# Optimization experiments

Measured on AMD Instinct MI355X. Metric: run time of the kernel, lower is better.

## Reference

```python
import jax, jax.numpy as jnp
import numpy as np

B, N, D, H, K, NH = 4096, 2048, 1024, 4096, 5, 8
HD = D // NH  # head dim


def setup_inputs() -> dict:
    key = jax.random.key(0)
    ks = jax.random.split(key, 12)
    s_d = np.float32(1.0 / np.sqrt(D))
    s_h = np.float32(1.0 / np.sqrt(H))
    rn = lambda k, sh, s: jax.random.normal(k, sh, dtype=jnp.float32) * s
    return {
        "morph0": jax.random.normal(ks[0], (B, D), dtype=jnp.float32),
        "stored_morph0": jax.random.normal(ks[1], (N, D), dtype=jnp.float32),
        "stored_morph1": jax.random.normal(ks[2], (N, D), dtype=jnp.float32),
        "wq": rn(ks[3], (D, D), s_d), "bq": jnp.zeros((D,), jnp.float32),
        "wk": rn(ks[4], (D, D), s_d), "bk": jnp.zeros((D,), jnp.float32),
        "wv": rn(ks[5], (D, D), s_d), "bv": jnp.zeros((D,), jnp.float32),
        "wo": rn(ks[6], (D, D), s_d), "bo": jnp.zeros((D,), jnp.float32),
        "w1": rn(ks[7], (H, D), s_d), "b1": jnp.zeros((H,), jnp.float32),
        "w2": rn(ks[8], (H, H), s_h), "b2": jnp.zeros((H,), jnp.float32),
        "w3": rn(ks[9], (D, H), s_h), "b3": jnp.zeros((D,), jnp.float32),
    }


def _l2norm(x):
    # F.normalize(dim=1): x / max(||x||, eps)
    n = jnp.sqrt(jnp.sum(x * x, axis=-1, keepdims=True))
    return x / jnp.maximum(n, 1e-12)


def reference(morph0, stored_morph0, stored_morph1,
              wq, bq, wk, bk, wv, bv, wo, bo,
              w1, b1, w2, b2, w3, b3):
    # ---- retrieve similar patterns: cosine sim + topk + fused gather-subtract ----
    qn = _l2norm(morph0)                       # [B, D]
    sn = _l2norm(stored_morph0)                # [N, D]
    sim = qn @ sn.T                            # [B, N]
    _, top_idx = jax.lax.top_k(sim, K)         # [B, K]
    evo = stored_morph1 - stored_morph0        # [N, D]
    selected = jnp.take(evo, top_idx, axis=0)  # [B, K, D] evolution vectors

    # ---- torch.nn.MultiheadAttention(D, 8, batch_first=True), eval mode ----
    q = (morph0 @ wq.T + bq).reshape(B, 1, NH, HD)      # [B, 1, NH, HD]
    k = (selected @ wk.T + bk).reshape(B, K, NH, HD)    # [B, K, NH, HD]
    v = (selected @ wv.T + bv).reshape(B, K, NH, HD)
    scores = jnp.einsum('bqhd,bkhd->bhqk', q, k) / np.float32(np.sqrt(HD))  # [B, NH, 1, K]
    attn = jax.nn.softmax(scores, axis=-1)
    ctx = jnp.einsum('bhqk,bkhd->bqhd', attn, v).reshape(B, 1, D)
    context = (ctx @ wo.T + bo)[:, 0, :]                # [B, D]
    attn_weights = attn.mean(axis=1)                    # [B, 1, K] (avg over heads)

    # ---- evolution net (dropout inactive in eval) + residual ----
    x = morph0 + context
    h1 = jax.nn.relu(x @ w1.T + b1)
    h2 = jax.nn.relu(h1 @ w2.T + b2)
    predicted = morph0 + (h2 @ w3.T + b3)
    return predicted, attn_weights
```

## Files before the change

### kernel.cpp

```cpp
#include <hip/hip_runtime.h>
#include <hip/hip_bf16.h>
#include <math.h>

typedef __bf16 bf16_t;
typedef __bf16 bf16x4 __attribute__((ext_vector_type(4)));
typedef __bf16 bf16x8 __attribute__((ext_vector_type(8)));
typedef float  f32x4  __attribute__((ext_vector_type(4)));

#define BB 4096
#define NN 2048
#define DD 1024
#define HH 4096
#define KSEL 5
#define NHEAD 8

__device__ __forceinline__ unsigned short bfbits(float f) {
  return __builtin_bit_cast(unsigned short, (bf16_t)f);
}

__device__ __forceinline__ void gload_lds16(const void* g, void* l) {
  __builtin_amdgcn_global_load_lds(
      (const __attribute__((address_space(1))) void*)g,
      (__attribute__((address_space(3))) void*)l, 16, 0, 0);
}

__device__ __forceinline__ ushort4 cvt4(float4 x) {
  ushort4 o;
  o.x = bfbits(x.x); o.y = bfbits(x.y); o.z = bfbits(x.z); o.w = bfbits(x.w);
  return o;
}

#define P_M0   1048576
#define P_S0   1572864
#define P_EVO  2097152
#define P_WQ   2359296
#define P_WKV  2883584
#define P_WO   3145728
#define P_W1   4194304
#define P_W2   8388608
#define P_W3   9437184
#define P_BKV  9437696
__global__ void __launch_bounds__(256)
prep_k(const float4* __restrict__ m0, const float4* __restrict__ s0,
       const float4* __restrict__ s1,
       const float4* __restrict__ wq, const float4* __restrict__ wk,
       const float4* __restrict__ wv, const float4* __restrict__ wo,
       const float4* __restrict__ w1, const float4* __restrict__ w2,
       const float4* __restrict__ w3,
       const float4* __restrict__ bk, const float4* __restrict__ bv,
       ushort4* __restrict__ m0b, ushort4* __restrict__ s0b,
       ushort4* __restrict__ evo,
       ushort4* __restrict__ wqb, ushort4* __restrict__ wkvb,
       ushort4* __restrict__ wob,
       ushort4* __restrict__ w1b, ushort4* __restrict__ w2b,
       ushort4* __restrict__ w3b, float4* __restrict__ bkv,
       double* __restrict__ rnd)
{
  __shared__ double red[256];
  const int tid = threadIdx.x;
  if (blockIdx.x >= 2048) {
    int n = blockIdx.x - 2048;
    float4 x = s0[(size_t)n * 256 + tid];
    double ss = (double)x.x * x.x + (double)x.y * x.y + (double)x.z * x.z + (double)x.w * x.w;
    red[tid] = ss; __syncthreads();
    for (int s = 128; s > 0; s >>= 1) {
      if (tid < s) red[tid] += red[tid + s];
      __syncthreads();
    }
    if (tid == 0) rnd[n] = 1.0 / fmax(sqrt(red[0]), 1e-12);
    return;
  }
  const int stride = 2048 * 256;
  for (int i = blockIdx.x * 256 + tid; i < P_BKV; i += stride) {
    if (i < P_M0) {
      m0b[i] = cvt4(m0[i]);
    } else if (i < P_S0) {
      int j = i - P_M0; s0b[j] = cvt4(s0[j]);
    } else if (i < P_EVO) {
      int j = i - P_S0;
      float4 a = s0[j], b = s1[j];
      float4 d; d.x = b.x - a.x; d.y = b.y - a.y; d.z = b.z - a.z; d.w = b.w - a.w;
      evo[j] = cvt4(d);
    } else if (i < P_WQ) {
      int j = i - P_EVO; wqb[j] = cvt4(wq[j]);
    } else if (i < P_WKV) {
      int j = i - P_WQ;
      wkvb[j] = cvt4(j < 262144 ? wk[j] : wv[j - 262144]);
    } else if (i < P_WO) {
      int j = i - P_WKV; wob[j] = cvt4(wo[j]);
    } else if (i < P_W1) {
      int j = i - P_WO; w1b[j] = cvt4(w1[j]);
    } else if (i < P_W2) {
      int j = i - P_W1; w2b[j] = cvt4(w2[j]);
    } else if (i < P_W3) {
      int j = i - P_W2; w3b[j] = cvt4(w3[j]);
    } else {
      int j = i - P_W3;
      bkv[j] = (j < 256) ? bk[j] : bv[j - 256];
    }
  }
}

template<bool RELU, bool RESID, bool OUTBF16>
__global__ void __launch_bounds__(256)
gemm_bt(const bf16_t* __restrict__ A, const bf16_t* __restrict__ Bw,
        const float* __restrict__ bias, const float* __restrict__ resid,
        float* __restrict__ outf, bf16_t* __restrict__ outb,
        int M, int Nn, int Kk)
{
  __shared__ alignas(16) bf16_t At[2][4096];
  __shared__ alignas(16) bf16_t Bt[2][4096];
  const int tid = threadIdx.x;
  const int wave = tid >> 6, lane = tid & 63;
  const int wm = wave >> 1, wn = wave & 1;
  const int bm = blockIdx.y << 7, bn = blockIdx.x << 7;
  const int ln15 = lane & 15, ln4 = lane >> 4;

  const int srow  = (wave << 4) + (lane >> 2);
  const int scolb = (((lane & 3) ^ ((lane >> 3) & 3)) << 4);
  const char* pA0 = (const char*)A  + (size_t)(bm + srow) * Kk * 2 + scolb;
  const char* pA1 = (const char*)A  + (size_t)(bm + srow + 64) * Kk * 2 + scolb;
  const char* pB0 = (const char*)Bw + (size_t)(bn + srow) * Kk * 2 + scolb;
  const char* pB1 = (const char*)Bw + (size_t)(bn + srow + 64) * Kk * 2 + scolb;

  f32x4 zero = {0.f, 0.f, 0.f, 0.f};
  f32x4 acc[4][4];
  #pragma unroll
  for (int i = 0; i < 4; ++i)
    #pragma unroll
    for (int j = 0; j < 4; ++j) acc[i][j] = zero;

  const int rslot = (ln4 ^ ((ln15 >> 1) & 3)) << 3;
  const int fAoff = ((wm << 6) + ln15) * 32 + rslot;
  const int fBoff = ((wn << 6) + ln15) * 32 + rslot;

  const int nt = Kk >> 5;
  {
    char* lA = (char*)At[0] + (wave << 10);
    char* lB = (char*)Bt[0] + (wave << 10);
    gload_lds16(pA0, lA);
    gload_lds16(pA1, lA + 4096);
    gload_lds16(pB0, lB);
    gload_lds16(pB1, lB + 4096);
  }
  __syncthreads();

  for (int t = 0; t < nt; ++t) {
    const int cur = t & 1;
    if (t + 1 < nt) {
      size_t kb = (size_t)(t + 1) << 6;
      char* lA = (char*)At[cur ^ 1] + (wave << 10);
      char* lB = (char*)Bt[cur ^ 1] + (wave << 10);
      gload_lds16(pA0 + kb, lA);
      gload_lds16(pA1 + kb, lA + 4096);
      gload_lds16(pB0 + kb, lB);
      gload_lds16(pB1 + kb, lB + 4096);
    }
    bf16x8 av[4], bv[4];
    #pragma unroll
    for (int i = 0; i < 4; ++i) av[i] = *(const bf16x8*)(&At[cur][fAoff + i * 512]);
    #pragma unroll
    for (int j = 0; j < 4; ++j) bv[j] = *(const bf16x8*)(&Bt[cur][fBoff + j * 512]);
    #pragma unroll
    for (int i = 0; i < 4; ++i)
      #pragma unroll
      for (int j = 0; j < 4; ++j)
        acc[i][j] = __builtin_amdgcn_mfma_f32_16x16x32_bf16(av[i], bv[j], acc[i][j], 0, 0, 0);
    __syncthreads();
  }

  const int r0 = bm + (wm << 6) + ((lane >> 4) << 2);
  const int c0 = bn + (wn << 6) + ln15;
  #pragma unroll
  for (int i = 0; i < 4; ++i) {
    #pragma unroll
    for (int j = 0; j < 4; ++j) {
      #pragma unroll
      for (int r = 0; r < 4; ++r) {
        int row = r0 + i * 16 + r;
        int col = c0 + j * 16;
        size_t o = (size_t)row * Nn + col;
        float v = acc[i][j][r];
        if (bias)  v += bias[col];
        if (RESID) v += resid[o];
        if (RELU)  v = fmaxf(v, 0.f);
        if (OUTBF16) outb[o] = (bf16_t)v;
        else         outf[o] = v;
      }
    }
  }
}

template<bool RELU>
__global__ void __launch_bounds__(512, 2)
gemm8(const bf16_t* __restrict__ A, const bf16_t* __restrict__ Bw,
      const float* __restrict__ bias, bf16_t* __restrict__ outb,
      int Nn, int Kk, int nbx)
{
  __shared__ alignas(16) bf16_t As[2][2][8192];
  __shared__ alignas(16) bf16_t Bs[2][2][8192];
  const int lane = threadIdx.x & 63, wv = threadIdx.x >> 6;
  const int wm = wv >> 2, wn = wv & 3;
  const int ln15 = lane & 15, ln4 = lane >> 4;

  const int nwg = gridDim.x;
  const int q = nwg >> 3, r = nwg & 7;
  const int xcd = blockIdx.x & 7, loc = blockIdx.x >> 3;
  const int swz = (xcd < r ? xcd * (q + 1) : r * (q + 1) + (xcd - r) * q) + loc;
  const int bm = (swz / nbx) << 8;
  const int bn = (swz % nbx) << 8;

  const int NT = Kk >> 6;

  f32x4 acc[8][4];
  f32x4 zero = {0.f, 0.f, 0.f, 0.f};
  #pragma unroll
  for (int i = 0; i < 8; ++i)
    #pragma unroll
    for (int j = 0; j < 4; ++j) acc[i][j] = zero;

  auto stA = [&](int mh, int buf, int kt) {
    #pragma unroll
    for (int u = 0; u < 2; ++u) {
      int lr = u * 64 + wv * 8 + (lane >> 3);
      int gr = ((lr >> 6) << 7) | (mh << 6) | (lr & 63);
      int slot = (lane & 7) ^ (lr & 7);
      gload_lds16(A + (size_t)(bm + gr) * Kk + kt * 64 + slot * 8,
                  (char*)&As[buf][mh][0] + (u * 64 + wv * 8) * 128);
    }
  };
  auto stB = [&](int nh, int buf, int kt) {
    #pragma unroll
    for (int u = 0; u < 2; ++u) {
      int lr = u * 64 + wv * 8 + (lane >> 3);
      int gr = ((lr >> 5) << 6) | (nh << 5) | (lr & 31);
      int slot = (lane & 7) ^ (lr & 7);
      gload_lds16(Bw + (size_t)(bn + gr) * Kk + kt * 64 + slot * 8,
                  (char*)&Bs[buf][nh][0] + (u * 64 + wv * 8) * 128);
    }
  };

  stB(0, 0, 0); stA(1, 0, 0); stB(1, 0, 0); stA(0, 0, 0);
  stB(0, 1, 1); stA(1, 1, 1); stB(1, 1, 1);
  asm volatile("s_waitcnt vmcnt(6)" ::: "memory");
  __builtin_amdgcn_s_barrier();

#define RD_A(MH, BF)                                                              \
    _Pragma("unroll") for (int mi = 0; mi < 4; ++mi)                              \
      _Pragma("unroll") for (int kk = 0; kk < 2; ++kk) {                          \
        const int lr = wm * 64 + mi * 16 + ln15;                                  \
        avv[mi][kk] = *(const bf16x8*)((const char*)&As[BF][MH][0] + lr * 128 +   \
                                       ((((kk << 2) | ln4) ^ (ln15 & 7)) << 4));  \
      }
#define RD_B(NH, BF)                                                              \
    _Pragma("unroll") for (int nj = 0; nj < 2; ++nj)                              \
      _Pragma("unroll") for (int kk = 0; kk < 2; ++kk) {                          \
        const int lr = wn * 32 + nj * 16 + ln15;                                  \
        bvv[nj][kk] = *(const bf16x8*)((const char*)&Bs[BF][NH][0] + lr * 128 +   \
                                       ((((kk << 2) | ln4) ^ (ln15 & 7)) << 4));  \
      }
#define GATE                                                                      \
    __builtin_amdgcn_s_barrier();                                                 \
    asm volatile("s_waitcnt lgkmcnt(0)" ::: "memory");                            \
    __builtin_amdgcn_sched_barrier(0);
#define MMA(MH, NH)                                                               \
    __builtin_amdgcn_s_setprio(1);                                                \
    _Pragma("unroll") for (int kk = 0; kk < 2; ++kk)                              \
      _Pragma("unroll") for (int mi = 0; mi < 4; ++mi)                            \
        _Pragma("unroll") for (int nj = 0; nj < 2; ++nj)                          \
          acc[(MH)*4+mi][(NH)*2+nj] = __builtin_amdgcn_mfma_f32_16x16x32_bf16(    \
              avv[mi][kk], bvv[nj][kk], acc[(MH)*4+mi][(NH)*2+nj], 0, 0, 0);      \
    __builtin_amdgcn_s_setprio(0);                                                \
    __builtin_amdgcn_s_barrier();

  for (int base = 0; base < NT; base += 2) {
    const bool more = (base + 2 < NT);
    bf16x8 avv[4][2], bvv[2][2];

    RD_A(0, 0); RD_B(0, 0);
    stA(0, 1, base + 1);
    asm volatile("s_waitcnt lgkmcnt(8)");
    GATE; MMA(0, 0);
    RD_A(1, 0);
    if (more) stB(0, 0, base + 2);
    GATE; MMA(1, 0);
    RD_B(1, 0);
    if (more) stA(1, 0, base + 2);
    GATE; MMA(1, 1);
    RD_A(0, 0);
    if (more) {
      stB(1, 0, base + 2);
      asm volatile("s_waitcnt vmcnt(6)" ::: "memory");
    } else {
      asm volatile("s_waitcnt vmcnt(0)" ::: "memory");
    }
    GATE; MMA(0, 1);

    RD_A(0, 1); RD_B(0, 1);
    if (more) stA(0, 0, base + 2);
    asm volatile("s_waitcnt lgkmcnt(8)");
    GATE; MMA(0, 0);
    RD_A(1, 1);
    if (more) stB(0, 1, base + 3);
    GATE; MMA(1, 0);
    RD_B(1, 1);
    if (more) stA(1, 1, base + 3);
    GATE; MMA(1, 1);
    RD_A(0, 1);
    if (more) stB(1, 1, base + 3);
    asm volatile("s_waitcnt vmcnt(6)" ::: "memory");
    GATE; MMA(0, 1);
  }
#undef RD_A
#undef RD_B
#undef GATE
#undef MMA

  #pragma unroll
  for (int am = 0; am < 8; ++am) {
    #pragma unroll
    for (int an = 0; an < 4; ++an) {
      #pragma unroll
      for (int rr = 0; rr < 4; ++rr) {
        int row = bm + wm * 128 + (am >> 2) * 64 + (am & 3) * 16 + (lane >> 4) * 4 + rr;
        int col = bn + wn * 64 + (an >> 1) * 32 + (an & 1) * 16 + ln15;
        float v = acc[am][an][rr] + bias[col];
        if (RELU) v = fmaxf(v, 0.f);
        outb[(size_t)row * Nn + col] = (bf16_t)v;
      }
    }
  }
}

__global__ void __launch_bounds__(256)
topk_refine_k(const float* __restrict__ sim, const double* __restrict__ rnd,
              const float* __restrict__ m0, const float* __restrict__ s0,
              int* __restrict__ topidx)
{
  __shared__ float vals[NN];
  __shared__ float rv[256];
  __shared__ int   ri[256];
  __shared__ int   c8[8];
  __shared__ double dred[256];
  __shared__ double dvals[8];
  const int b = blockIdx.x, tid = threadIdx.x;
  for (int t = 0; t < NN / 256; ++t) {
    int i = tid + t * 256;
    vals[i] = sim[(size_t)b * NN + i] * (float)rnd[i];
  }
  __syncthreads();
  for (int p = 0; p < 8; ++p) {
    float bvv = -INFINITY; int bi = NN;
    for (int t = 0; t < NN / 256; ++t) {
      int i = tid + t * 256;
      float v = vals[i];
      if (v > bvv) { bvv = v; bi = i; }
    }
    rv[tid] = bvv; ri[tid] = bi;
    __syncthreads();
    for (int s = 128; s > 0; s >>= 1) {
      if (tid < s) {
        float v2 = rv[tid + s]; int i2 = ri[tid + s];
        if (v2 > rv[tid] || (v2 == rv[tid] && i2 < ri[tid])) { rv[tid] = v2; ri[tid] = i2; }
      }
      __syncthreads();
    }
    if (tid == 0) {
      int wsel = ri[0];
      c8[p] = wsel;
      vals[wsel] = -INFINITY;
    }
    __syncthreads();
  }
  int cs[8];
  #pragma unroll
  for (int j = 0; j < 8; ++j) cs[j] = c8[j];
  const float* qrow = m0 + (size_t)b * DD;
  double part[8];
  #pragma unroll
  for (int j = 0; j < 8; ++j) part[j] = 0.0;
  for (int d = tid; d < DD; d += 256) {
    double qd = (double)qrow[d];
    #pragma unroll
    for (int j = 0; j < 8; ++j)
      part[j] += qd * (double)s0[(size_t)cs[j] * DD + d];
  }
  for (int j = 0; j < 8; ++j) {
    dred[tid] = part[j]; __syncthreads();
    for (int s = 128; s > 0; s >>= 1) {
      if (tid < s) dred[tid] += dred[tid + s];
      __syncthreads();
    }
    if (tid == 0) dvals[j] = dred[0] * rnd[cs[j]];
    __syncthreads();
  }
  if (tid == 0) {
    bool used[8] = {false,false,false,false,false,false,false,false};
    for (int p = 0; p < KSEL; ++p) {
      int best = -1;
      for (int j = 0; j < 8; ++j) {
        if (used[j]) continue;
        if (best < 0 || dvals[j] > dvals[best] ||
            (dvals[j] == dvals[best] && cs[j] < cs[best])) best = j;
      }
      used[best] = true;
      topidx[b * KSEL + p] = cs[best];
    }
  }
}

__global__ void __launch_bounds__(256)
attn_k(const bf16_t* __restrict__ q, const bf16_t* __restrict__ eKV,
       const int* __restrict__ tidx,
       bf16_t* __restrict__ ctx, float* __restrict__ attn_out)
{
  __shared__ float aw[NHEAD][KSEL];
  const int b = blockIdx.x, t = threadIdx.x;
  const int d0 = t << 2;
  int idx[KSEL];
  #pragma unroll
  for (int j = 0; j < KSEL; ++j) idx[j] = tidx[b * KSEL + j];

  bf16x4 qv = *(const bf16x4*)(q + (size_t)b * DD + d0);
  float s[KSEL];
  #pragma unroll
  for (int j = 0; j < KSEL; ++j) {
    bf16x4 kv = *(const bf16x4*)(eKV + (size_t)idx[j] * 2048 + d0);
    float p = (float)qv[0] * (float)kv[0] + (float)qv[1] * (float)kv[1]
            + (float)qv[2] * (float)kv[2] + (float)qv[3] * (float)kv[3];
    #pragma unroll
    for (int m = 16; m > 0; m >>= 1) p += __shfl_xor(p, m);
    s[j] = p * 0.08838834764831845f;
  }
  float mx = s[0];
  #pragma unroll
  for (int j = 1; j < KSEL; ++j) mx = fmaxf(mx, s[j]);
  float e[KSEL], sum = 0.f;
  #pragma unroll
  for (int j = 0; j < KSEL; ++j) { e[j] = expf(s[j] - mx); sum += e[j]; }
  float inv = 1.f / sum;

  float c0 = 0.f, c1 = 0.f, c2 = 0.f, c3 = 0.f;
  #pragma unroll
  for (int j = 0; j < KSEL; ++j) {
    float a = e[j] * inv;
    bf16x4 vv = *(const bf16x4*)(eKV + (size_t)idx[j] * 2048 + 1024 + d0);
    c0 += a * (float)vv[0]; c1 += a * (float)vv[1];
    c2 += a * (float)vv[2]; c3 += a * (float)vv[3];
    if ((t & 31) == 0) aw[t >> 5][j] = a;
  }
  bf16x4 co; co[0] = (bf16_t)c0; co[1] = (bf16_t)c1; co[2] = (bf16_t)c2; co[3] = (bf16_t)c3;
  *(bf16x4*)(ctx + (size_t)b * DD + d0) = co;
  __syncthreads();
  if (t < KSEL) {
    float m = 0.f;
    #pragma unroll
    for (int hh = 0; hh < NHEAD; ++hh) m += aw[hh][t];
    attn_out[(size_t)b * KSEL + t] = m * 0.125f;
  }
}

extern "C" void kernel_launch(void* const* d_in, const int* in_sizes, int n_in,
                              void* d_out, int out_size, void* d_ws, size_t ws_size,
                              hipStream_t stream) {
  (void)in_sizes; (void)n_in; (void)out_size; (void)ws_size;
  const float* morph0 = (const float*)d_in[0];
  const float* s0     = (const float*)d_in[1];
  const float* s1     = (const float*)d_in[2];
  const float* wq = (const float*)d_in[3];  const float* bq = (const float*)d_in[4];
  const float* wk = (const float*)d_in[5];  const float* bk = (const float*)d_in[6];
  const float* wv = (const float*)d_in[7];  const float* bv = (const float*)d_in[8];
  const float* wo = (const float*)d_in[9];  const float* bo = (const float*)d_in[10];
  const float* w1 = (const float*)d_in[11]; const float* b1 = (const float*)d_in[12];
  const float* w2 = (const float*)d_in[13]; const float* b2 = (const float*)d_in[14];
  const float* w3 = (const float*)d_in[15]; const float* b3 = (const float*)d_in[16];

  char* ws = (char*)d_ws;
  size_t off = 0;
  auto alloc = [&](size_t bytes) { char* p = ws + off; off += (bytes + 255) & ~(size_t)255; return p; };

  float*  sim  = (float*) alloc((size_t)BB * NN * 4);
  bf16_t* m0b  = (bf16_t*)alloc((size_t)BB * DD * 2);
  bf16_t* s0b  = (bf16_t*)alloc((size_t)NN * DD * 2);
  bf16_t* evo  = (bf16_t*)alloc((size_t)NN * DD * 2);
  double* rnd  = (double*)alloc((size_t)NN * 8);
  int*    tidx = (int*)   alloc((size_t)BB * KSEL * 4);
  bf16_t* qb   = (bf16_t*)alloc((size_t)BB * DD * 2);
  bf16_t* eKVb = (bf16_t*)alloc((size_t)NN * 2048 * 2);
  bf16_t* ctxb = (bf16_t*)alloc((size_t)BB * DD * 2);
  bf16_t* xb   = (bf16_t*)alloc((size_t)BB * DD * 2);
  bf16_t* wqb  = (bf16_t*)alloc((size_t)DD * DD * 2);
  bf16_t* wkvb = (bf16_t*)alloc((size_t)2048 * DD * 2);
  bf16_t* wob  = (bf16_t*)alloc((size_t)DD * DD * 2);
  bf16_t* w1b  = (bf16_t*)alloc((size_t)HH * DD * 2);
  bf16_t* w2b  = (bf16_t*)alloc((size_t)HH * HH * 2);
  bf16_t* w3b  = (bf16_t*)alloc((size_t)DD * HH * 2);
  float*  bkv  = (float*) alloc((size_t)2048 * 4);
  bf16_t* h2b  = (bf16_t*)alloc((size_t)BB * HH * 2);
  bf16_t* h1b  = (bf16_t*)sim;
  float*  attn_out = (float*)d_out + (size_t)BB * DD;

  prep_k<<<dim3(4096), dim3(256), 0, stream>>>(
      (const float4*)morph0, (const float4*)s0, (const float4*)s1,
      (const float4*)wq, (const float4*)wk, (const float4*)wv, (const float4*)wo,
      (const float4*)w1, (const float4*)w2, (const float4*)w3,
      (const float4*)bk, (const float4*)bv,
      (ushort4*)m0b, (ushort4*)s0b, (ushort4*)evo,
      (ushort4*)wqb, (ushort4*)wkvb, (ushort4*)wob,
      (ushort4*)w1b, (ushort4*)w2b, (ushort4*)w3b, (float4*)bkv, rnd);

  gemm_bt<false,false,false><<<dim3(NN/128, BB/128), dim3(256), 0, stream>>>(
      m0b, s0b, nullptr, nullptr, sim, nullptr, BB, NN, DD);
  topk_refine_k<<<dim3(BB), dim3(256), 0, stream>>>(sim, rnd, morph0, s0, tidx);

  gemm_bt<false,false,true><<<dim3(DD/128, BB/128), dim3(256), 0, stream>>>(
      m0b, wqb, bq, nullptr, nullptr, qb, BB, DD, DD);
  gemm_bt<false,false,true><<<dim3(2048/128, NN/128), dim3(256), 0, stream>>>(
      evo, wkvb, bkv, nullptr, nullptr, eKVb, NN, 2048, DD);

  attn_k<<<dim3(BB), dim3(256), 0, stream>>>(qb, eKVb, tidx, ctxb, attn_out);

  gemm_bt<false,true,true><<<dim3(DD/128, BB/128), dim3(256), 0, stream>>>(
      ctxb, wob, bo, morph0, nullptr, xb, BB, DD, DD);

  gemm8<true><<<dim3((BB/256)*(HH/256)), dim3(512), 0, stream>>>(
      xb, w1b, b1, h1b, HH, DD, HH/256);
  gemm8<true><<<dim3((BB/256)*(HH/256)), dim3(512), 0, stream>>>(
      h1b, w2b, b2, h2b, HH, HH, HH/256);
  gemm_bt<false,true,false><<<dim3(DD/128, BB/128), dim3(256), 0, stream>>>(
      h2b, w3b, b3, morph0, (float*)d_out, nullptr, BB, DD, HH);
}
```

Before: 506.7 us.

## Replace iterative top-8 selection with per-thread sorted lists and merge tree

Result: slower. 559.2 us (+10.4%).

```diff
diff --git a/kernel.cpp b/kernel.cpp
--- a/kernel.cpp
+++ b/kernel.cpp
@@ -240,8 +240,8 @@
     }
   };
 
-  stB(0, 0, 0); stA(1, 0, 0); stB(1, 0, 0); stA(0, 0, 0);
-  stB(0, 1, 1); stA(1, 1, 1); stB(1, 1, 1);
+  stB(0, 0, 0); stB(1, 0, 0); stA(1, 0, 0); stA(0, 0, 0);
+  stB(0, 1, 1); stB(1, 1, 1); stA(1, 1, 1);
   asm volatile("s_waitcnt vmcnt(6)" ::: "memory");
   __builtin_amdgcn_s_barrier();
 
@@ -252,64 +252,62 @@
         avv[mi][kk] = *(const bf16x8*)((const char*)&As[BF][MH][0] + lr * 128 +   \
                                        ((((kk << 2) | ln4) ^ (ln15 & 7)) << 4));  \
       }
-#define RD_B(NH, BF)                                                              \
+#define RD_B(BV, NH, BF)                                                          \
     _Pragma("unroll") for (int nj = 0; nj < 2; ++nj)                              \
       _Pragma("unroll") for (int kk = 0; kk < 2; ++kk) {                          \
         const int lr = wn * 32 + nj * 16 + ln15;                                  \
-        bvv[nj][kk] = *(const bf16x8*)((const char*)&Bs[BF][NH][0] + lr * 128 +   \
-                                       ((((kk << 2) | ln4) ^ (ln15 & 7)) << 4));  \
+        BV[nj][kk] = *(const bf16x8*)((const char*)&Bs[BF][NH][0] + lr * 128 +    \
+                                      ((((kk << 2) | ln4) ^ (ln15 & 7)) << 4));   \
       }
 #define GATE                                                                      \
     __builtin_amdgcn_s_barrier();                                                 \
     asm volatile("s_waitcnt lgkmcnt(0)" ::: "memory");                            \
     __builtin_amdgcn_sched_barrier(0);
-#define MMA(MH, NH)                                                               \
+#define MMA(MH, NH, BV)                                                           \
     __builtin_amdgcn_s_setprio(1);                                                \
     _Pragma("unroll") for (int kk = 0; kk < 2; ++kk)                              \
       _Pragma("unroll") for (int mi = 0; mi < 4; ++mi)                            \
         _Pragma("unroll") for (int nj = 0; nj < 2; ++nj)                          \
           acc[(MH)*4+mi][(NH)*2+nj] = __builtin_amdgcn_mfma_f32_16x16x32_bf16(    \
-              avv[mi][kk], bvv[nj][kk], acc[(MH)*4+mi][(NH)*2+nj], 0, 0, 0);      \
+              avv[mi][kk], BV[nj][kk], acc[(MH)*4+mi][(NH)*2+nj], 0, 0, 0);       \
     __builtin_amdgcn_s_setprio(0);                                                \
     __builtin_amdgcn_s_barrier();
 
   for (int base = 0; base < NT; base += 2) {
     const bool more = (base + 2 < NT);
-    bf16x8 avv[4][2], bvv[2][2];
-
-    RD_A(0, 0); RD_B(0, 0);
+    bf16x8 avv[4][2], bv0[2][2], bv1[2][2];
+
+    RD_A(0, 0); RD_B(bv0, 0, 0);
     stA(0, 1, base + 1);
     asm volatile("s_waitcnt lgkmcnt(8)");
-    GATE; MMA(0, 0);
+    GATE; MMA(0, 0, bv0);
+    RD_B(bv1, 1, 0);
+    if (more) stB(0, 0, base + 2);
+    GATE; MMA(0, 1, bv1);
     RD_A(1, 0);
-    if (more) stB(0, 0, base + 2);
-    GATE; MMA(1, 0);
-    RD_B(1, 0);
-    if (more) stA(1, 0, base + 2);
-    GATE; MMA(1, 1);
-    RD_A(0, 0);
+    if (more) stB(1, 0, base + 2);
+    GATE; MMA(1, 1, bv1);
     if (more) {
-      stB(1, 0, base + 2);
+      stA(1, 0, base + 2);
       asm volatile("s_waitcnt vmcnt(6)" ::: "memory");
     } else {
       asm volatile("s_waitcnt vmcnt(0)" ::: "memory");
     }
-    GATE; MMA(0, 1);
-
-    RD_A(0, 1); RD_B(0, 1);
+    GATE; MMA(1, 0, bv0);
+
+    RD_A(0, 1); RD_B(bv0, 0, 1);
     if (more) stA(0, 0, base + 2);
     asm volatile("s_waitcnt lgkmcnt(8)");
-    GATE; MMA(0, 0);
+    GATE; MMA(0, 0, bv0);
+    RD_B(bv1, 1, 1);
+    if (more) stB(0, 1, base + 3);
+    GATE; MMA(0, 1, bv1);
     RD_A(1, 1);
-    if (more) stB(0, 1, base + 3);
-    GATE; MMA(1, 0);
-    RD_B(1, 1);
+    if (more) stB(1, 1, base + 3);
+    GATE; MMA(1, 1, bv1);
     if (more) stA(1, 1, base + 3);
-    GATE; MMA(1, 1);
-    RD_A(0, 1);
-    if (more) stB(1, 1, base + 3);
     asm volatile("s_waitcnt vmcnt(6)" ::: "memory");
-    GATE; MMA(0, 1);
+    GATE; MMA(1, 0, bv0);
   }
 #undef RD_A
 #undef RD_B
@@ -337,44 +335,54 @@
               const float* __restrict__ m0, const float* __restrict__ s0,
               int* __restrict__ topidx)
 {
-  __shared__ float vals[NN];
-  __shared__ float rv[256];
-  __shared__ int   ri[256];
-  __shared__ int   c8[8];
+  __shared__ float  lv[2][256][8];
+  __shared__ int    li[2][256][8];
   __shared__ double dred[256];
   __shared__ double dvals[8];
   const int b = blockIdx.x, tid = threadIdx.x;
-  for (int t = 0; t < NN / 256; ++t) {
+
+  float tv[8]; int ti[8];
+  #pragma unroll
+  for (int p = 0; p < 8; ++p) { tv[p] = -INFINITY; ti[p] = NN; }
+  #pragma unroll
+  for (int t = 0; t < 8; ++t) {
     int i = tid + t * 256;
-    vals[i] = sim[(size_t)b * NN + i] * (float)rnd[i];
-  }
+    float v = sim[(size_t)b * NN + i] * (float)rnd[i];
+    int   ix = i;
+    #pragma unroll
+    for (int p = 0; p < 8; ++p) {
+      bool better = (v > tv[p]) || (v == tv[p] && ix < ti[p]);
+      if (better) {
+        float sv = tv[p]; int si = ti[p];
+        tv[p] = v; ti[p] = ix; v = sv; ix = si;
+      }
+    }
+  }
+  #pragma unroll
+  for (int p = 0; p < 8; ++p) { lv[0][tid][p] = tv[p]; li[0][tid][p] = ti[p]; }
   __syncthreads();
-  for (int p = 0; p < 8; ++p) {
-    float bvv = -INFINITY; int bi = NN;
-    for (int t = 0; t < NN / 256; ++t) {
-      int i = tid + t * 256;
-      float v = vals[i];
-      if (v > bvv) { bvv = v; bi = i; }
-    }
-    rv[tid] = bvv; ri[tid] = bi;
+
+  int cur = 0;
+  for (int s = 128; s > 0; s >>= 1) {
+    if (tid < s) {
+      int ia = 0, ib = 0;
+      #pragma unroll
+      for (int p = 0; p < 8; ++p) {
+        float va = lv[cur][tid][ia],     vb = lv[cur][tid + s][ib];
+        int   ja = li[cur][tid][ia],     jb = li[cur][tid + s][ib];
+        bool ta = (va > vb) || (va == vb && ja < jb);
+        lv[cur ^ 1][tid][p] = ta ? va : vb;
+        li[cur ^ 1][tid][p] = ta ? ja : jb;
+        if (ta) ++ia; else ++ib;
+      }
+    }
     __syncthreads();
-    for (int s = 128; s > 0; s >>= 1) {
-      if (tid < s) {
-        float v2 = rv[tid + s]; int i2 = ri[tid + s];
-        if (v2 > rv[tid] || (v2 == rv[tid] && i2 < ri[tid])) { rv[tid] = v2; ri[tid] = i2; }
-      }
-      __syncthreads();
-    }
-    if (tid == 0) {
-      int wsel = ri[0];
-      c8[p] = wsel;
-      vals[wsel] = -INFINITY;
-    }
-    __syncthreads();
+    cur ^= 1;
   }
   int cs[8];
   #pragma unroll
-  for (int j = 0; j < 8; ++j) cs[j] = c8[j];
+  for (int j = 0; j < 8; ++j) cs[j] = li[cur][0][j];
+
   const float* qrow = m0 + (size_t)b * DD;
   double part[8];
   #pragma unroll
```

## Restructure gemm8 main loop into single-barrier double-buffered schedule with sched_group_barriers

Applied to the files above, without the earlier changes.

Measured after the change: 499.2 us. Within noise of the previous version (-1.5%).

```diff
diff --git a/kernel.cpp b/kernel.cpp
--- a/kernel.cpp
+++ b/kernel.cpp
@@ -191,6 +191,9 @@
   }
 }
 
+#define SGB_M(n) __builtin_amdgcn_sched_group_barrier(0x008, n, 0)
+#define SGB_D(n) __builtin_amdgcn_sched_group_barrier(0x100, n, 0)
+#define SGB_V(n) __builtin_amdgcn_sched_group_barrier(0x020, n, 0)
 template<bool RELU>
 __global__ void __launch_bounds__(512, 2)
 gemm8(const bf16_t* __restrict__ A, const bf16_t* __restrict__ Bw,
@@ -240,81 +243,92 @@
     }
   };
 
-  stB(0, 0, 0); stA(1, 0, 0); stB(1, 0, 0); stA(0, 0, 0);
-  stB(0, 1, 1); stA(1, 1, 1); stB(1, 1, 1);
-  asm volatile("s_waitcnt vmcnt(6)" ::: "memory");
+  stA(0, 0, 0); stA(1, 0, 0); stB(0, 0, 0); stB(1, 0, 0);
+  asm volatile("s_waitcnt vmcnt(0)" ::: "memory");
   __builtin_amdgcn_s_barrier();
-
-#define RD_A(MH, BF)                                                              \
+  __builtin_amdgcn_sched_barrier(0);
+
+#define RD_A4(AV, MH, KK, BF)                                                     \
+    _Pragma("unroll") for (int mi = 0; mi < 4; ++mi) {                            \
+      const int lr = wm * 64 + mi * 16 + ln15;                                    \
+      AV[mi] = *(const bf16x8*)((const char*)&As[BF][MH][0] + lr * 128 +          \
+                                (((((KK) << 2) | ln4) ^ (ln15 & 7)) << 4));       \
+    }
+#define RD_B2(BV, NH, KK, BF)                                                     \
+    _Pragma("unroll") for (int nj = 0; nj < 2; ++nj) {                            \
+      const int lr = wn * 32 + nj * 16 + ln15;                                    \
+      BV[nj] = *(const bf16x8*)((const char*)&Bs[BF][NH][0] + lr * 128 +          \
+                                (((((KK) << 2) | ln4) ^ (ln15 & 7)) << 4));       \
+    }
+#define MMA8(AV, BV, MH, NH)                                                      \
     _Pragma("unroll") for (int mi = 0; mi < 4; ++mi)                              \
-      _Pragma("unroll") for (int kk = 0; kk < 2; ++kk) {                          \
-        const int lr = wm * 64 + mi * 16 + ln15;                                  \
-        avv[mi][kk] = *(const bf16x8*)((const char*)&As[BF][MH][0] + lr * 128 +   \
-                                       ((((kk << 2) | ln4) ^ (ln15 & 7)) << 4));  \
-      }
-#define RD_B(NH, BF)                                                              \
-    _Pragma("unroll") for (int nj = 0; nj < 2; ++nj)                              \
-      _Pragma("unroll") for (int kk = 0; kk < 2; ++kk) {                          \
-        const int lr = wn * 32 + nj * 16 + ln15;                                  \
-        bvv[nj][kk] = *(const bf16x8*)((const char*)&Bs[BF][NH][0] + lr * 128 +   \
-                                       ((((kk << 2) | ln4) ^ (ln15 & 7)) << 4));  \
-      }
-#define GATE                                                                      \
-    __builtin_amdgcn_s_barrier();                                                 \
-    asm volatile("s_waitcnt lgkmcnt(0)" ::: "memory");                            \
+      _Pragma("unroll") for (int nj = 0; nj < 2; ++nj)                            \
+        acc[(MH)*4+mi][(NH)*2+nj] = __builtin_amdgcn_mfma_f32_16x16x32_bf16(      \
+            AV[mi], BV[nj], acc[(MH)*4+mi][(NH)*2+nj], 0, 0, 0);
+
+  for (int t = 0; t < NT - 1; ++t) {
+    const int cur = t & 1, nb = cur ^ 1;
+    bf16x8 ae[4], ao[4], b0k0[2], b1k0[2], b0k1[2], b1k1[2];
+
+    RD_A4(ae, 0, 0, cur); RD_B2(b0k0, 0, 0, cur);
+    stA(0, nb, t + 1); stB(0, nb, t + 1);
+    SGB_D(6); SGB_V(4);
+    RD_B2(b1k0, 1, 0, cur); RD_A4(ao, 1, 0, cur);
+    MMA8(ae, b0k0, 0, 0);
+    #pragma unroll
+    for (int i = 0; i < 6; ++i) { SGB_M(1); SGB_D(1); }
+    SGB_M(2);
+    MMA8(ae, b1k0, 0, 1);
+    SGB_M(8);
+    RD_A4(ae, 0, 1, cur);
+    MMA8(ao, b1k0, 1, 1);
+    #pragma unroll
+    for (int i = 0; i < 4; ++i) { SGB_M(2); SGB_D(1); }
+    RD_B2(b1k1, 1, 1, cur);
+    stA(1, nb, t + 1); stB(1, nb, t + 1);
+    MMA8(ao, b0k0, 1, 0);
+    SGB_M(1); SGB_D(1); SGB_M(1); SGB_D(1);
+    #pragma unroll
+    for (int i = 0; i < 4; ++i) { SGB_M(1); SGB_V(1); }
+    SGB_M(2);
+    RD_B2(b0k1, 0, 1, cur);
+    MMA8(ae, b1k1, 0, 1);
+    SGB_M(3); SGB_D(1); SGB_M(3); SGB_D(1); SGB_M(2);
+    RD_A4(ao, 1, 1, cur);
+    MMA8(ae, b0k1, 0, 0);
+    #pragma unroll
+    for (int i = 0; i < 4; ++i) { SGB_M(2); SGB_D(1); }
+    MMA8(ao, b0k1, 1, 0);
+    SGB_M(8);
+    MMA8(ao, b1k1, 1, 1);
+    SGB_M(8);
+    asm volatile("s_waitcnt vmcnt(0)" ::: "memory");
     __builtin_amdgcn_sched_barrier(0);
-#define MMA(MH, NH)                                                               \
-    __builtin_amdgcn_s_setprio(1);                                                \
-    _Pragma("unroll") for (int kk = 0; kk < 2; ++kk)                              \
-      _Pragma("unroll") for (int mi = 0; mi < 4; ++mi)                            \
-        _Pragma("unroll") for (int nj = 0; nj < 2; ++nj)                          \
-          acc[(MH)*4+mi][(NH)*2+nj] = __builtin_amdgcn_mfma_f32_16x16x32_bf16(    \
-              avv[mi][kk], bvv[nj][kk], acc[(MH)*4+mi][(NH)*2+nj], 0, 0, 0);      \
-    __builtin_amdgcn_s_setprio(0);                                                \
     __builtin_amdgcn_s_barrier();
-
-  for (int base = 0; base < NT; base += 2) {
-    const bool more = (base + 2 < NT);
-    bf16x8 avv[4][2], bvv[2][2];
-
-    RD_A(0, 0); RD_B(0, 0);
-    stA(0, 1, base + 1);
-    asm volatile("s_waitcnt lgkmcnt(8)");
-    GATE; MMA(0, 0);
-    RD_A(1, 0);
-    if (more) stB(0, 0, base + 2);
-    GATE; MMA(1, 0);
-    RD_B(1, 0);
-    if (more) stA(1, 0, base + 2);
-    GATE; MMA(1, 1);
-    RD_A(0, 0);
-    if (more) {
-      stB(1, 0, base + 2);
-      asm volatile("s_waitcnt vmcnt(6)" ::: "memory");
-    } else {
-      asm volatile("s_waitcnt vmcnt(0)" ::: "memory");
-    }
-    GATE; MMA(0, 1);
-
-    RD_A(0, 1); RD_B(0, 1);
-    if (more) stA(0, 0, base + 2);
-    asm volatile("s_waitcnt lgkmcnt(8)");
-    GATE; MMA(0, 0);
-    RD_A(1, 1);
-    if (more) stB(0, 1, base + 3);
-    GATE; MMA(1, 0);
-    RD_B(1, 1);
-    if (more) stA(1, 1, base + 3);
-    GATE; MMA(1, 1);
-    RD_A(0, 1);
-    if (more) stB(1, 1, base + 3);
-    asm volatile("s_waitcnt vmcnt(6)" ::: "memory");
-    GATE; MMA(0, 1);
-  }
-#undef RD_A
-#undef RD_B
-#undef GATE
-#undef MMA
+    __builtin_amdgcn_sched_barrier(0);
+  }
+
+  {
+    const int cur = (NT - 1) & 1;
+    bf16x8 ae[4], ao[4], b0k0[2], b1k0[2], b0k1[2], b1k1[2];
+    RD_A4(ae, 0, 0, cur); RD_B2(b0k0, 0, 0, cur);
+    RD_B2(b1k0, 1, 0, cur); RD_A4(ao, 1, 0, cur);
+    MMA8(ae, b0k0, 0, 0);
+    MMA8(ae, b1k0, 0, 1);
+    RD_A4(ae, 0, 1, cur);
+    MMA8(ao, b1k0, 1, 1);
+    RD_B2(b1k1, 1, 1, cur);
+    MMA8(ao, b0k0, 1, 0);
+    RD_B2(b0k1, 0, 1, cur);
+    MMA8(ae, b1k1, 0, 1);
+    RD_A4(ao, 1, 1, cur);
+    MMA8(ae, b0k1, 0, 0);
+    MMA8(ao, b0k1, 1, 0);
+    MMA8(ao, b1k1, 1, 1);
+  }
+#undef RD_A4
+#undef RD_B2
+#undef MMA8
 
   #pragma unroll
   for (int am = 0; am < 8; ++am) {
@@ -331,6 +345,9 @@
     }
   }
 }
+#undef SGB_M
+#undef SGB_D
+#undef SGB_V
 
 __global__ void __launch_bounds__(256)
 topk_refine_k(const float* __restrict__ sim, const double* __restrict__ rnd,
```
